# Optimization experiments

Hardware: AMD Instinct MI355X
Metric: run time of the kernel (lower is better)

The kernel has to match this reference:

```python
import jax, jax.numpy as jnp
import numpy as np

N = 100_000      # nodes
E = 1_600_000    # edges (avg degree 16)
D_IN = 128
D_H = 128
D_P = 128
D_OUT = 64


def setup_inputs() -> dict:
    key = jax.random.key(0)
    ks = jax.random.split(key, 10)
    x = jax.random.normal(ks[0], (N, D_IN), dtype=jnp.float32)
    edge_index = jax.random.randint(ks[1], (2, E), 0, N, dtype=jnp.int64)
    # Mix_Pass layer 0: Linear(in->hidden, bias=False) + separate bias (zero-init)
    W1 = jax.random.normal(ks[2], (D_H, D_IN), dtype=jnp.float32) * 0.05
    b1 = jnp.zeros((D_H,), dtype=jnp.float32)
    # Mix_Pass layer 1: hidden->hidden
    W2 = jax.random.normal(ks[3], (D_H, D_H), dtype=jnp.float32) * 0.05
    b2 = jnp.zeros((D_H,), dtype=jnp.float32)
    # projection MLP
    fcW1 = jax.random.normal(ks[4], (D_P, D_H), dtype=jnp.float32) * 0.05
    fcb1 = jnp.zeros((D_P,), dtype=jnp.float32)
    fcW2 = jax.random.normal(ks[5], (D_OUT, D_P), dtype=jnp.float32) * 0.05
    fcb2 = jnp.zeros((D_OUT,), dtype=jnp.float32)
    return dict(x=x, edge_index=edge_index, W1=W1, b1=b1, W2=W2, b2=b2,
                fcW1=fcW1, fcb1=fcb1, fcW2=fcW2, fcb2=fcb2)


def _gcn_norm_with_self_loops(edge_index, n_nodes):
    # add_self_loops then gcn_norm (sym, improved=False, loops already added)
    loop = jnp.arange(n_nodes, dtype=edge_index.dtype)
    row = jnp.concatenate([edge_index[0], loop])  # source
    col = jnp.concatenate([edge_index[1], loop])  # target
    ew = jnp.ones(row.shape[0], dtype=jnp.float32)
    deg = jax.ops.segment_sum(ew, col, num_segments=n_nodes)
    dinv = jnp.where(deg > 0, jax.lax.rsqrt(deg), 0.0)
    return row, col, dinv[row] * ew * dinv[col]


def _mix_pass(z, W, b, row, col, ew, n_nodes):
    z = z @ W.T                                   # [N, out]
    msg = ew[:, None] * z[row]                    # gather source feats, scale
    out = jax.ops.segment_sum(msg, col, num_segments=n_nodes)  # scatter-add
    return out + b


def reference(x, edge_index, W1, b1, W2, b2, fcW1, fcb1, fcW2, fcb2):
    n_nodes = x.shape[0]
    row, col, ew = _gcn_norm_with_self_loops(edge_index, n_nodes)
    # dropout is identity in eval mode
    z = jax.nn.relu(_mix_pass(x, W1, b1, row, col, ew, n_nodes))
    zs = _mix_pass(z, W2, b2, row, col, ew, n_nodes)
    # project: elu(fc1) -> log_softmax(fc2)
    h = jax.nn.elu(zs @ fcW1.T + fcb1)
    res = jax.nn.log_softmax(h @ fcW2.T + fcb2, axis=1)
    return zs, res
```

## Files before the change

### kernel.cpp

```cpp
#include <hip/hip_runtime.h>
#include <hip/hip_bf16.h>

typedef __bf16 bf16_t;
typedef bf16_t bf16x8 __attribute__((ext_vector_type(8)));
typedef bf16_t bf16x4 __attribute__((ext_vector_type(4)));
typedef bf16_t bf16x2 __attribute__((ext_vector_type(2)));
typedef float f32x4 __attribute__((ext_vector_type(4)));

#define DEG_CAP 64
#define BKT_SHIFT 8
#define BKT_CAP 6144
#define EPT 8

__device__ __forceinline__ void cvt4(const float* __restrict__ s, bf16_t* __restrict__ d, int i) {
    f32x4 v = ((const f32x4*)s)[i];
    bf16x4 o;
#pragma unroll
    for (int j = 0; j < 4; ++j) o[j] = (bf16_t)v[j];
    ((bf16x4*)d)[i] = o;
}

__global__ void setup_k(const float* xf, bf16_t* Xbf, int nx4,
                        const float* W1f, bf16_t* W1b,
                        const float* W2f, bf16_t* W2b,
                        const float* fW1f, bf16_t* fW1b,
                        const float* fW2f, bf16_t* fW2b,
                        int* gbcnt, int NB, int* yzero) {
    int i = blockIdx.x * blockDim.x + threadIdx.x;
    if (i < nx4) { cvt4(xf, Xbf, i); return; }
    i -= nx4;
    if (i < 4096) { cvt4(W1f, W1b, i); return; }
    i -= 4096;
    if (i < 4096) { cvt4(W2f, W2b, i); return; }
    i -= 4096;
    if (i < 4096) { cvt4(fW1f, fW1b, i); return; }
    i -= 4096;
    if (i < 2048) { cvt4(fW2f, fW2b, i); return; }
    i -= 2048;
    if (i < NB) { gbcnt[i] = 0; return; }
    i -= NB;
    if (i < 64) yzero[i] = 0;
}

__global__ __launch_bounds__(256) void bucket_scatter_k(const int* __restrict__ ei,
                                                        int* __restrict__ gbcnt,
                                                        unsigned* __restrict__ grec,
                                                        int E, int N) {
    __shared__ int hist[512];
    __shared__ int base[512];
    const int tid = threadIdx.x;
    const int NB = (N + 255) >> BKT_SHIFT;
    for (int i = tid; i < NB; i += 256) hist[i] = 0;
    __syncthreads();

    const int wave = tid >> 6, lane = tid & 63;
    const int e0 = blockIdx.x * (256 * EPT) + wave * (64 * EPT) + lane;
    const bool i64 = (ei[1] == 0) & (ei[3] == 0) & (ei[5] == 0) & (ei[7] == 0);

    unsigned rec[EPT];
    int lof[EPT];
    int bk[EPT];
#pragma unroll
    for (int j = 0; j < EPT; ++j) {
        int e = e0 + j * 64;
        bk[j] = -1;
        if (e < E) {
            int r, c;
            if (i64) { r = ei[2 * e]; c = ei[2 * E + 2 * e]; }
            else     { r = ei[e];     c = ei[E + e]; }
            r = ((unsigned)r < (unsigned)N) ? r : 0;
            c = ((unsigned)c < (unsigned)N) ? c : 0;
            int b = c >> BKT_SHIFT;
            rec[j] = ((unsigned)r << BKT_SHIFT) | (unsigned)(c & 255);
            bk[j] = b;
            lof[j] = atomicAdd(&hist[b], 1);
        }
    }
    __syncthreads();
    for (int i = tid; i < NB; i += 256)
        base[i] = hist[i] ? atomicAdd(&gbcnt[i], hist[i]) : 0;
    __syncthreads();
#pragma unroll
    for (int j = 0; j < EPT; ++j) {
        if (bk[j] >= 0) {
            int pos = base[bk[j]] + lof[j];
            if (pos < BKT_CAP)
                grec[(size_t)bk[j] * BKT_CAP + pos] = rec[j];
        }
    }
}

__global__ __launch_bounds__(256) void bucket_place_k(const int* __restrict__ gbcnt,
                                                      const unsigned* __restrict__ grec,
                                                      int* __restrict__ cnt,
                                                      int* __restrict__ srcx, int N) {
    __shared__ int lcnt[256];
    const int b = blockIdx.x, tid = threadIdx.x;
    lcnt[tid] = 0;
    __syncthreads();
    int ne = gbcnt[b];
    if (ne > BKT_CAP) ne = BKT_CAP;
    const unsigned* rp = grec + (size_t)b * BKT_CAP;
    const int node0 = b << BKT_SHIFT;
    for (int i = tid; i < ne; i += 256) {
        unsigned rec = rp[i];
        int cl = rec & 255;
        int r  = rec >> BKT_SHIFT;
        int p = atomicAdd(&lcnt[cl], 1);
        if (p < DEG_CAP) srcx[(size_t)(node0 + cl) * DEG_CAP + p] = r;
    }
    __syncthreads();
    int node = node0 + tid;
    if (node < N) {
        int c = lcnt[tid];
        cnt[node] = c;
        int cc = (c < DEG_CAP) ? c : DEG_CAP;
        int pe = (cc + 15) & ~15;
        if (pe > DEG_CAP) pe = DEG_CAP;
        int* s = srcx + (size_t)node * DEG_CAP;
        for (int p = cc; p < pe; ++p) s[p] = N;
    }
}

template <int RELU, int WF32>
__global__ __launch_bounds__(256) void gather_k(const bf16_t* __restrict__ Y,
                                                const int* __restrict__ cnt,
                                                const int* __restrict__ srcx,
                                                const float* __restrict__ bias,
                                                bf16_t* __restrict__ out,
                                                float* __restrict__ out2, int n) {
    int node0 = (blockIdx.x * 4 + (threadIdx.x >> 6)) * 2;
    if (node0 >= n) return;
    const int lane = threadIdx.x & 63;
    const int l16 = lane & 15;
    const int quad = lane >> 4;
    const bool has1 = node0 + 1 < n;
    const int node1 = has1 ? node0 + 1 : n;

    int2 cc = *(const int2*)(cnt + node0);
    int c0 = cc.x;
    int c1 = has1 ? cc.y : 0;
    float di0 = rsqrtf((float)c0 + 1.0f);
    float di1 = rsqrtf((float)c1 + 1.0f);
    int cg0 = (c0 < DEG_CAP) ? c0 : DEG_CAP;
    int cg1 = (c1 < DEG_CAP) ? c1 : DEG_CAP;
    int nb0 = (cg0 + 15) & ~15;
    int nb1 = (cg1 + 15) & ~15;
    int nbm = nb0 > nb1 ? nb0 : nb1;

    const int* sl0 = srcx + (size_t)node0 * DEG_CAP;
    const int* sl1 = srcx + (size_t)node1 * DEG_CAP;
    const bf16_t* Yl = Y + l16 * 8;

    bf16x8 ys0 = *(const bf16x8*)(Yl + (size_t)node0 * 128);
    bf16x8 ys1 = *(const bf16x8*)(Yl + (size_t)node1 * 128);

    float acc0[8], acc1[8];
#pragma unroll
    for (int j = 0; j < 8; ++j) { acc0[j] = 0.f; acc1[j] = 0.f; }

    for (int e = 0; e < nbm; e += 16) {
        int4 sq0, sq1;
        bool d0 = e < nb0, d1 = e < nb1;
        if (d0) sq0 = *(const int4*)(sl0 + e + quad * 4);
        if (d1) sq1 = *(const int4*)(sl1 + e + quad * 4);
        if (d0) {
            bf16x8 y0 = *(const bf16x8*)(Yl + (size_t)sq0.x * 128);
            bf16x8 y1 = *(const bf16x8*)(Yl + (size_t)sq0.y * 128);
            bf16x8 y2 = *(const bf16x8*)(Yl + (size_t)sq0.z * 128);
            bf16x8 y3 = *(const bf16x8*)(Yl + (size_t)sq0.w * 128);
#pragma unroll
            for (int j = 0; j < 8; ++j)
                acc0[j] += (float)y0[j] + (float)y1[j] + (float)y2[j] + (float)y3[j];
        }
        if (d1) {
            bf16x8 y0 = *(const bf16x8*)(Yl + (size_t)sq1.x * 128);
            bf16x8 y1 = *(const bf16x8*)(Yl + (size_t)sq1.y * 128);
            bf16x8 y2 = *(const bf16x8*)(Yl + (size_t)sq1.z * 128);
            bf16x8 y3 = *(const bf16x8*)(Yl + (size_t)sq1.w * 128);
#pragma unroll
            for (int j = 0; j < 8; ++j)
                acc1[j] += (float)y0[j] + (float)y1[j] + (float)y2[j] + (float)y3[j];
        }
    }

#pragma unroll
    for (int j = 0; j < 8; ++j) {
        acc0[j] += __shfl_xor(acc0[j], 16);
        acc0[j] += __shfl_xor(acc0[j], 32);
        acc1[j] += __shfl_xor(acc1[j], 16);
        acc1[j] += __shfl_xor(acc1[j], 32);
    }

    f32x4 b0 = ((const f32x4*)bias)[l16 * 2];
    f32x4 b1 = ((const f32x4*)bias)[l16 * 2 + 1];
    float v0[8], v1[8];
#pragma unroll
    for (int j = 0; j < 8; ++j) {
        float bb = (j < 4) ? b0[j & 3] : b1[j & 3];
        v0[j] = di0 * ((float)ys0[j] + acc0[j]) + bb;
        v1[j] = di1 * ((float)ys1[j] + acc1[j]) + bb;
        if (RELU) { v0[j] = fmaxf(v0[j], 0.f); v1[j] = fmaxf(v1[j], 0.f); }
    }

    if (quad == 0) {
        bf16x8 o;
#pragma unroll
        for (int j = 0; j < 8; ++j) o[j] = (bf16_t)v0[j];
        *(bf16x8*)(out + (size_t)node0 * 128 + l16 * 8) = o;
    } else if (quad == 1 && has1) {
        bf16x8 o;
#pragma unroll
        for (int j = 0; j < 8; ++j) o[j] = (bf16_t)v1[j];
        *(bf16x8*)(out + (size_t)node1 * 128 + l16 * 8) = o;
    }
    if (WF32) {
        if (quad == 2) {
            f32x4 w = {v0[0], v0[1], v0[2], v0[3]};
            *(f32x4*)(out2 + (size_t)node0 * 128 + l16 * 8) = w;
        } else if (quad == 3) {
            f32x4 w = {v0[4], v0[5], v0[6], v0[7]};
            *(f32x4*)(out2 + (size_t)node0 * 128 + l16 * 8 + 4) = w;
        } else if (quad == 0 && has1) {
            f32x4 w = {v1[0], v1[1], v1[2], v1[3]};
            *(f32x4*)(out2 + (size_t)node1 * 128 + l16 * 8) = w;
        } else if (quad == 1 && has1) {
            f32x4 w = {v1[4], v1[5], v1[6], v1[7]};
            *(f32x4*)(out2 + (size_t)node1 * 128 + l16 * 8 + 4) = w;
        }
    }
}

template <int OC, int MODE, int MT>
__global__ __launch_bounds__(256) void gemm_k(const bf16_t* __restrict__ A,
                                              const bf16_t* __restrict__ W,
                                              const float* __restrict__ bias,
                                              const int* __restrict__ cnt,
                                              bf16_t* __restrict__ out,
                                              float* __restrict__ outf, int nrows) {
    const int lane = threadIdx.x & 63;
    const int wave = threadIdx.x >> 6;
    const int l16 = lane & 15;
    const int quad = lane >> 4;
    constexpr int NT = OC / 16;
    const int ntiles = (nrows + 15) >> 4;
    const int t0 = (blockIdx.x * 4 + wave) * MT;
    if (t0 >= ntiles) return;

    f32x4 acc[MT][NT];
#pragma unroll
    for (int mt = 0; mt < MT; ++mt)
#pragma unroll
        for (int n = 0; n < NT; ++n) acc[mt][n] = (f32x4){0.f, 0.f, 0.f, 0.f};

    const bf16_t* arow[MT];
#pragma unroll
    for (int mt = 0; mt < MT; ++mt) {
        int r = t0 * 16 + mt * 16 + l16;
        if (r > nrows - 1) r = nrows - 1;
        arow[mt] = A + (size_t)r * 128 + quad * 8;
    }
    const bf16_t* wrow = W + (size_t)l16 * 128 + quad * 8;

#pragma unroll
    for (int kt = 0; kt < 4; ++kt) {
        bf16x8 a[MT];
#pragma unroll
        for (int mt = 0; mt < MT; ++mt) a[mt] = *(const bf16x8*)(arow[mt] + kt * 32);
#pragma unroll
        for (int n = 0; n < NT; ++n) {
            bf16x8 b = *(const bf16x8*)(wrow + (size_t)n * 2048 + kt * 32);
#pragma unroll
            for (int mt = 0; mt < MT; ++mt)
                acc[mt][n] = __builtin_amdgcn_mfma_f32_16x16x32_bf16(a[mt], b, acc[mt][n], 0, 0, 0);
        }
    }

#pragma unroll
    for (int mt = 0; mt < MT; ++mt) {
        int m0 = (t0 + mt) * 16;
        if (m0 >= nrows) break;
#pragma unroll
        for (int r = 0; r < 4; ++r) {
            int row = m0 + quad * 4 + r;
            if (row < nrows) {
                float sc = rsqrtf((float)cnt[row] + 1.0f);
#pragma unroll
                for (int n = 0; n < NT; ++n)
                    out[(size_t)row * OC + n * 16 + l16] = (bf16_t)(sc * acc[mt][n][r]);
            }
        }
    }
}

#define LDW 136
__global__ __launch_bounds__(256) void head_k(const bf16_t* __restrict__ A,
                                              const bf16_t* __restrict__ W1,
                                              const float* __restrict__ b1,
                                              const bf16_t* __restrict__ W2,
                                              const float* __restrict__ b2,
                                              float* __restrict__ outf, int nrows) {
    __shared__ bf16_t hl[4][16 * LDW];
    const int lane = threadIdx.x & 63;
    const int wave = threadIdx.x >> 6;
    const int l16 = lane & 15;
    const int quad = lane >> 4;
    const int ntiles = (nrows + 15) >> 4;
    int t = blockIdx.x * 4 + wave;
    const bool live = t < ntiles;
    if (!live) t = ntiles - 1;
    const int m0 = t * 16;

    f32x4 acc[8];
#pragma unroll
    for (int n = 0; n < 8; ++n) acc[n] = (f32x4){0.f, 0.f, 0.f, 0.f};
    int r0 = m0 + l16;
    if (r0 > nrows - 1) r0 = nrows - 1;
    const bf16_t* arow = A + (size_t)r0 * 128 + quad * 8;
    const bf16_t* wrow = W1 + (size_t)l16 * 128 + quad * 8;
#pragma unroll
    for (int kt = 0; kt < 4; ++kt) {
        bf16x8 a = *(const bf16x8*)(arow + kt * 32);
#pragma unroll
        for (int n = 0; n < 8; ++n) {
            bf16x8 b = *(const bf16x8*)(wrow + (size_t)n * 2048 + kt * 32);
            acc[n] = __builtin_amdgcn_mfma_f32_16x16x32_bf16(a, b, acc[n], 0, 0, 0);
        }
    }
    bf16_t* hw = hl[wave];
#pragma unroll
    for (int n = 0; n < 8; ++n) {
        float bb = b1[n * 16 + l16];
#pragma unroll
        for (int r = 0; r < 4; ++r) {
            float v = acc[n][r] + bb;
            v = (v > 0.0f) ? v : (expf(v) - 1.0f);
            hw[(quad * 4 + r) * LDW + n * 16 + l16] = (bf16_t)v;
        }
    }
    __syncthreads();

    f32x4 acc2[4];
#pragma unroll
    for (int n = 0; n < 4; ++n) acc2[n] = (f32x4){0.f, 0.f, 0.f, 0.f};
    const bf16_t* hrow = hw + l16 * LDW + quad * 8;
    const bf16_t* wrow2 = W2 + (size_t)l16 * 128 + quad * 8;
#pragma unroll
    for (int kt = 0; kt < 4; ++kt) {
        bf16x8 a = *(const bf16x8*)(hrow + kt * 32);
#pragma unroll
        for (int n = 0; n < 4; ++n) {
            bf16x8 b = *(const bf16x8*)(wrow2 + (size_t)n * 2048 + kt * 32);
            acc2[n] = __builtin_amdgcn_mfma_f32_16x16x32_bf16(a, b, acc2[n], 0, 0, 0);
        }
    }
#pragma unroll
    for (int r = 0; r < 4; ++r) {
        float v[4];
#pragma unroll
        for (int n = 0; n < 4; ++n) v[n] = acc2[n][r] + b2[n * 16 + l16];
        float mx = v[0];
#pragma unroll
        for (int n = 1; n < 4; ++n) mx = fmaxf(mx, v[n]);
#pragma unroll
        for (int m = 8; m >= 1; m >>= 1) mx = fmaxf(mx, __shfl_xor(mx, m));
        float s = 0.0f;
#pragma unroll
        for (int n = 0; n < 4; ++n) s += expf(v[n] - mx);
#pragma unroll
        for (int m = 8; m >= 1; m >>= 1) s += __shfl_xor(s, m);
        float lse = mx + logf(s);
        int row = m0 + quad * 4 + r;
        if (live && row < nrows)
#pragma unroll
            for (int n = 0; n < 4; ++n)
                outf[(size_t)row * 64 + n * 16 + l16] = v[n] - lse;
    }
}

extern "C" void kernel_launch(void* const* d_in, const int* in_sizes, int n_in,
                              void* d_out, int out_size, void* d_ws, size_t ws_size,
                              hipStream_t stream) {
    const float* xf    = (const float*)d_in[0];
    const int*   ei    = (const int*)d_in[1];
    const float* W1f   = (const float*)d_in[2];
    const float* b1f   = (const float*)d_in[3];
    const float* W2f   = (const float*)d_in[4];
    const float* b2f   = (const float*)d_in[5];
    const float* fcW1f = (const float*)d_in[6];
    const float* fcb1f = (const float*)d_in[7];
    const float* fcW2f = (const float*)d_in[8];
    const float* fcb2f = (const float*)d_in[9];

    const int N = in_sizes[0] / 128;
    const int E = in_sizes[1] / 2;
    const int NB = (N + 255) >> BKT_SHIFT;

    float* zs_out  = (float*)d_out;
    float* res_out = (float*)d_out + (size_t)N * 128;

    char* ws = (char*)d_ws;
    size_t o = 0;
    auto carve = [&](size_t bytes) { void* p = ws + o; o = (o + bytes + 255) & ~255UL; return p; };
    int*      cnt   = (int*)carve((size_t)N * 4);
    int*      srcx  = (int*)carve((size_t)N * DEG_CAP * 4);
    bf16_t*   Xbf   = (bf16_t*)carve((size_t)N * 128 * 2);
    bf16_t*   Ybf   = (bf16_t*)carve((size_t)(N + 1) * 128 * 2);
    bf16_t*   W1b   = (bf16_t*)carve(128 * 128 * 2);
    bf16_t*   W2b   = (bf16_t*)carve(128 * 128 * 2);
    bf16_t*   fW1b  = (bf16_t*)carve(128 * 128 * 2);
    bf16_t*   fW2b  = (bf16_t*)carve(64 * 128 * 2);
    unsigned* grec  = (unsigned*)carve((size_t)NB * BKT_CAP * 4);
    int*      gbcnt = (int*)carve((size_t)NB * 4);

    const int B = 256;
    const int ntiles = (N + 15) / 16;
    const int gblocks = (ntiles + 7) / 8;
    const int hblocks = (ntiles + 3) / 4;
    const int nodeblocks = (N + 7) / 8;
    const int nx4 = N * 32;
    const int nsetup = nx4 + 4096 * 3 + 2048 + NB + 64;
    const int ablocks = (E + 256 * EPT - 1) / (256 * EPT);

    setup_k<<<(nsetup + B - 1) / B, B, 0, stream>>>(xf, Xbf, nx4, W1f, W1b, W2f, W2b,
                                                    fcW1f, fW1b, fcW2f, fW2b, gbcnt, NB,
                                                    (int*)(Ybf + (size_t)N * 128));
    bucket_scatter_k<<<ablocks, B, 0, stream>>>(ei, gbcnt, grec, E, N);
    bucket_place_k<<<NB, B, 0, stream>>>(gbcnt, grec, cnt, srcx, N);

    gemm_k<128, 0, 2><<<gblocks, B, 0, stream>>>(Xbf, W1b, nullptr, cnt, Ybf, nullptr, N);
    gather_k<1, 0><<<nodeblocks, B, 0, stream>>>(Ybf, cnt, srcx, b1f, Xbf, nullptr, N);

    gemm_k<128, 0, 2><<<gblocks, B, 0, stream>>>(Xbf, W2b, nullptr, cnt, Ybf, nullptr, N);
    gather_k<0, 1><<<nodeblocks, B, 0, stream>>>(Ybf, cnt, srcx, b2f, Xbf, zs_out, N);

    head_k<<<hblocks, B, 0, stream>>>(Xbf, fW1b, fcb1f, fW2b, fcb2f, res_out, N);
}
```

Before: 417.2 us.

## Fuse x fp32-to-bf16 conversion into first GEMM and simplify gather to one node per wave

```diff
diff --git a/kernel.cpp b/kernel.cpp
--- a/kernel.cpp
+++ b/kernel.cpp
@@ -6,11 +6,12 @@
 typedef bf16_t bf16x4 __attribute__((ext_vector_type(4)));
 typedef bf16_t bf16x2 __attribute__((ext_vector_type(2)));
 typedef float f32x4 __attribute__((ext_vector_type(4)));
+typedef float f32x2 __attribute__((ext_vector_type(2)));
 
 #define DEG_CAP 64
 #define BKT_SHIFT 8
 #define BKT_CAP 6144
-#define EPT 8
+#define EPT 16
 
 __device__ __forceinline__ void cvt4(const float* __restrict__ s, bf16_t* __restrict__ d, int i) {
     f32x4 v = ((const f32x4*)s)[i];
@@ -20,15 +21,12 @@
     ((bf16x4*)d)[i] = o;
 }
 
-__global__ void setup_k(const float* xf, bf16_t* Xbf, int nx4,
-                        const float* W1f, bf16_t* W1b,
+__global__ void setup_k(const float* W1f, bf16_t* W1b,
                         const float* W2f, bf16_t* W2b,
                         const float* fW1f, bf16_t* fW1b,
                         const float* fW2f, bf16_t* fW2b,
                         int* gbcnt, int NB, int* yzero) {
     int i = blockIdx.x * blockDim.x + threadIdx.x;
-    if (i < nx4) { cvt4(xf, Xbf, i); return; }
-    i -= nx4;
     if (i < 4096) { cvt4(W1f, W1b, i); return; }
     i -= 4096;
     if (i < 4096) { cvt4(W2f, W2b, i); return; }
@@ -116,6 +114,7 @@
         cnt[node] = c;
         int cc = (c < DEG_CAP) ? c : DEG_CAP;
         int pe = (cc + 15) & ~15;
+        if (pe < 16) pe = 16;
         if (pe > DEG_CAP) pe = DEG_CAP;
         int* s = srcx + (size_t)node * DEG_CAP;
         for (int p = cc; p < pe; ++p) s[p] = N;
@@ -129,115 +128,87 @@
                                                 const float* __restrict__ bias,
                                                 bf16_t* __restrict__ out,
                                                 float* __restrict__ out2, int n) {
-    int node0 = (blockIdx.x * 4 + (threadIdx.x >> 6)) * 2;
-    if (node0 >= n) return;
+    int node = blockIdx.x * 4 + (threadIdx.x >> 6);
+    if (node >= n) return;
     const int lane = threadIdx.x & 63;
     const int l16 = lane & 15;
     const int quad = lane >> 4;
-    const bool has1 = node0 + 1 < n;
-    const int node1 = has1 ? node0 + 1 : n;
-
-    int2 cc = *(const int2*)(cnt + node0);
-    int c0 = cc.x;
-    int c1 = has1 ? cc.y : 0;
-    float di0 = rsqrtf((float)c0 + 1.0f);
-    float di1 = rsqrtf((float)c1 + 1.0f);
-    int cg0 = (c0 < DEG_CAP) ? c0 : DEG_CAP;
-    int cg1 = (c1 < DEG_CAP) ? c1 : DEG_CAP;
-    int nb0 = (cg0 + 15) & ~15;
-    int nb1 = (cg1 + 15) & ~15;
-    int nbm = nb0 > nb1 ? nb0 : nb1;
-
-    const int* sl0 = srcx + (size_t)node0 * DEG_CAP;
-    const int* sl1 = srcx + (size_t)node1 * DEG_CAP;
+    const int* sl = srcx + (size_t)node * DEG_CAP + quad * 4;
     const bf16_t* Yl = Y + l16 * 8;
 
-    bf16x8 ys0 = *(const bf16x8*)(Yl + (size_t)node0 * 128);
-    bf16x8 ys1 = *(const bf16x8*)(Yl + (size_t)node1 * 128);
-
-    float acc0[8], acc1[8];
-#pragma unroll
-    for (int j = 0; j < 8; ++j) { acc0[j] = 0.f; acc1[j] = 0.f; }
-
-    for (int e = 0; e < nbm; e += 16) {
-        int4 sq0, sq1;
-        bool d0 = e < nb0, d1 = e < nb1;
-        if (d0) sq0 = *(const int4*)(sl0 + e + quad * 4);
-        if (d1) sq1 = *(const int4*)(sl1 + e + quad * 4);
-        if (d0) {
-            bf16x8 y0 = *(const bf16x8*)(Yl + (size_t)sq0.x * 128);
-            bf16x8 y1 = *(const bf16x8*)(Yl + (size_t)sq0.y * 128);
-            bf16x8 y2 = *(const bf16x8*)(Yl + (size_t)sq0.z * 128);
-            bf16x8 y3 = *(const bf16x8*)(Yl + (size_t)sq0.w * 128);
-#pragma unroll
-            for (int j = 0; j < 8; ++j)
-                acc0[j] += (float)y0[j] + (float)y1[j] + (float)y2[j] + (float)y3[j];
-        }
-        if (d1) {
-            bf16x8 y0 = *(const bf16x8*)(Yl + (size_t)sq1.x * 128);
-            bf16x8 y1 = *(const bf16x8*)(Yl + (size_t)sq1.y * 128);
-            bf16x8 y2 = *(const bf16x8*)(Yl + (size_t)sq1.z * 128);
-            bf16x8 y3 = *(const bf16x8*)(Yl + (size_t)sq1.w * 128);
-#pragma unroll
-            for (int j = 0; j < 8; ++j)
-                acc1[j] += (float)y0[j] + (float)y1[j] + (float)y2[j] + (float)y3[j];
-        }
-    }
-
+    int4 sq = *(const int4*)sl;
+    bf16x8 ys = *(const bf16x8*)(Yl + (size_t)node * 128);
+    int c = cnt[node];
+    float di = rsqrtf((float)c + 1.0f);
+    int cg = (c < DEG_CAP) ? c : DEG_CAP;
+    int nb = (cg + 15) & ~15;
+
+    f32x2 acc[4];
+#pragma unroll
+    for (int p = 0; p < 4; ++p) acc[p] = (f32x2){0.f, 0.f};
+
+#define ACC_ROW(s)                                                             \
+    {                                                                          \
+        bf16x8 yv = *(const bf16x8*)(Yl + (size_t)(s) * 128);                  \
+        uint4 u = *(const uint4*)&yv;                                          \
+        acc[0] += (f32x2){__uint_as_float(u.x << 16),                          \
+                          __uint_as_float(u.x & 0xFFFF0000u)};                 \
+        acc[1] += (f32x2){__uint_as_float(u.y << 16),                          \
+                          __uint_as_float(u.y & 0xFFFF0000u)};                 \
+        acc[2] += (f32x2){__uint_as_float(u.z << 16),                          \
+                          __uint_as_float(u.z & 0xFFFF0000u)};                 \
+        acc[3] += (f32x2){__uint_as_float(u.w << 16),                          \
+                          __uint_as_float(u.w & 0xFFFF0000u)};                 \
+    }
+
+    ACC_ROW(sq.x); ACC_ROW(sq.y); ACC_ROW(sq.z); ACC_ROW(sq.w);
+    for (int e = 16; e < nb; e += 16) {
+        int4 s2 = *(const int4*)(sl + e);
+        ACC_ROW(s2.x); ACC_ROW(s2.y); ACC_ROW(s2.z); ACC_ROW(s2.w);
+    }
+#undef ACC_ROW
+
+    float a[8];
+#pragma unroll
+    for (int p = 0; p < 4; ++p) { a[2 * p] = acc[p][0]; a[2 * p + 1] = acc[p][1]; }
 #pragma unroll
     for (int j = 0; j < 8; ++j) {
-        acc0[j] += __shfl_xor(acc0[j], 16);
-        acc0[j] += __shfl_xor(acc0[j], 32);
-        acc1[j] += __shfl_xor(acc1[j], 16);
-        acc1[j] += __shfl_xor(acc1[j], 32);
+        a[j] += __shfl_xor(a[j], 16);
+        a[j] += __shfl_xor(a[j], 32);
     }
 
     f32x4 b0 = ((const f32x4*)bias)[l16 * 2];
     f32x4 b1 = ((const f32x4*)bias)[l16 * 2 + 1];
-    float v0[8], v1[8];
+    float v[8];
 #pragma unroll
     for (int j = 0; j < 8; ++j) {
         float bb = (j < 4) ? b0[j & 3] : b1[j & 3];
-        v0[j] = di0 * ((float)ys0[j] + acc0[j]) + bb;
-        v1[j] = di1 * ((float)ys1[j] + acc1[j]) + bb;
-        if (RELU) { v0[j] = fmaxf(v0[j], 0.f); v1[j] = fmaxf(v1[j], 0.f); }
+        v[j] = di * ((float)ys[j] + a[j]) + bb;
+        if (RELU) v[j] = fmaxf(v[j], 0.f);
     }
 
     if (quad == 0) {
         bf16x8 o;
 #pragma unroll
-        for (int j = 0; j < 8; ++j) o[j] = (bf16_t)v0[j];
-        *(bf16x8*)(out + (size_t)node0 * 128 + l16 * 8) = o;
-    } else if (quad == 1 && has1) {
-        bf16x8 o;
-#pragma unroll
-        for (int j = 0; j < 8; ++j) o[j] = (bf16_t)v1[j];
-        *(bf16x8*)(out + (size_t)node1 * 128 + l16 * 8) = o;
+        for (int j = 0; j < 8; ++j) o[j] = (bf16_t)v[j];
+        *(bf16x8*)(out + (size_t)node * 128 + l16 * 8) = o;
     }
     if (WF32) {
-        if (quad == 2) {
-            f32x4 w = {v0[0], v0[1], v0[2], v0[3]};
-            *(f32x4*)(out2 + (size_t)node0 * 128 + l16 * 8) = w;
-        } else if (quad == 3) {
-            f32x4 w = {v0[4], v0[5], v0[6], v0[7]};
-            *(f32x4*)(out2 + (size_t)node0 * 128 + l16 * 8 + 4) = w;
-        } else if (quad == 0 && has1) {
-            f32x4 w = {v1[0], v1[1], v1[2], v1[3]};
-            *(f32x4*)(out2 + (size_t)node1 * 128 + l16 * 8) = w;
-        } else if (quad == 1 && has1) {
-            f32x4 w = {v1[4], v1[5], v1[6], v1[7]};
-            *(f32x4*)(out2 + (size_t)node1 * 128 + l16 * 8 + 4) = w;
-        }
-    }
-}
-
-template <int OC, int MODE, int MT>
-__global__ __launch_bounds__(256) void gemm_k(const bf16_t* __restrict__ A,
+        if (quad == 1) {
+            f32x4 w = {v[0], v[1], v[2], v[3]};
+            *(f32x4*)(out2 + (size_t)node * 128 + l16 * 8) = w;
+        } else if (quad == 2) {
+            f32x4 w = {v[4], v[5], v[6], v[7]};
+            *(f32x4*)(out2 + (size_t)node * 128 + l16 * 8 + 4) = w;
+        }
+    }
+}
+
+template <int OC, int MT, int AF32>
+__global__ __launch_bounds__(256) void gemm_k(const void* __restrict__ Av,
                                               const bf16_t* __restrict__ W,
-                                              const float* __restrict__ bias,
                                               const int* __restrict__ cnt,
-                                              bf16_t* __restrict__ out,
-                                              float* __restrict__ outf, int nrows) {
+                                              bf16_t* __restrict__ out, int nrows) {
     const int lane = threadIdx.x & 63;
     const int wave = threadIdx.x >> 6;
     const int l16 = lane & 15;
@@ -254,11 +225,13 @@
         for (int n = 0; n < NT; ++n) acc[mt][n] = (f32x4){0.f, 0.f, 0.f, 0.f};
 
     const bf16_t* arow[MT];
+    const float* afrow[MT];
 #pragma unroll
     for (int mt = 0; mt < MT; ++mt) {
         int r = t0 * 16 + mt * 16 + l16;
         if (r > nrows - 1) r = nrows - 1;
-        arow[mt] = A + (size_t)r * 128 + quad * 8;
+        if (AF32) afrow[mt] = (const float*)Av + (size_t)r * 128 + quad * 8;
+        else      arow[mt]  = (const bf16_t*)Av + (size_t)r * 128 + quad * 8;
     }
     const bf16_t* wrow = W + (size_t)l16 * 128 + quad * 8;
 
@@ -266,7 +239,19 @@
     for (int kt = 0; kt < 4; ++kt) {
         bf16x8 a[MT];
 #pragma unroll
-        for (int mt = 0; mt < MT; ++mt) a[mt] = *(const bf16x8*)(arow[mt] + kt * 32);
+        for (int mt = 0; mt < MT; ++mt) {
+            if (AF32) {
+                f32x4 lo = *(const f32x4*)(afrow[mt] + kt * 32);
+                f32x4 hi = *(const f32x4*)(afrow[mt] + kt * 32 + 4);
+#pragma unroll
+                for (int j = 0; j < 4; ++j) {
+                    a[mt][j] = (bf16_t)lo[j];
+                    a[mt][j + 4] = (bf16_t)hi[j];
+                }
+            } else {
+                a[mt] = *(const bf16x8*)(arow[mt] + kt * 32);
+            }
+        }
 #pragma unroll
         for (int n = 0; n < NT; ++n) {
             bf16x8 b = *(const bf16x8*)(wrow + (size_t)n * 2048 + kt * 32);
@@ -417,21 +402,20 @@
     const int ntiles = (N + 15) / 16;
     const int gblocks = (ntiles + 7) / 8;
     const int hblocks = (ntiles + 3) / 4;
-    const int nodeblocks = (N + 7) / 8;
-    const int nx4 = N * 32;
-    const int nsetup = nx4 + 4096 * 3 + 2048 + NB + 64;
+    const int nodeblocks = (N + 3) / 4;
+    const int nsetup = 4096 * 3 + 2048 + NB + 64;
     const int ablocks = (E + 256 * EPT - 1) / (256 * EPT);
 
-    setup_k<<<(nsetup + B - 1) / B, B, 0, stream>>>(xf, Xbf, nx4, W1f, W1b, W2f, W2b,
+    setup_k<<<(nsetup + B - 1) / B, B, 0, stream>>>(W1f, W1b, W2f, W2b,
                                                     fcW1f, fW1b, fcW2f, fW2b, gbcnt, NB,
                                                     (int*)(Ybf + (size_t)N * 128));
     bucket_scatter_k<<<ablocks, B, 0, stream>>>(ei, gbcnt, grec, E, N);
     bucket_place_k<<<NB, B, 0, stream>>>(gbcnt, grec, cnt, srcx, N);
 
-    gemm_k<128, 0, 2><<<gblocks, B, 0, stream>>>(Xbf, W1b, nullptr, cnt, Ybf, nullptr, N);
+    gemm_k<128, 2, 1><<<gblocks, B, 0, stream>>>((const void*)xf, W1b, cnt, Ybf, N);
     gather_k<1, 0><<<nodeblocks, B, 0, stream>>>(Ybf, cnt, srcx, b1f, Xbf, nullptr, N);
 
-    gemm_k<128, 0, 2><<<gblocks, B, 0, stream>>>(Xbf, W2b, nullptr, cnt, Ybf, nullptr, N);
+    gemm_k<128, 2, 0><<<gblocks, B, 0, stream>>>((const void*)Xbf, W2b, cnt, Ybf, N);
     gather_k<0, 1><<<nodeblocks, B, 0, stream>>>(Ybf, cnt, srcx, b2f, Xbf, zs_out, N);
 
     head_k<<<hblocks, B, 0, stream>>>(Xbf, fW1b, fcb1f, fW2b, fcb2f, res_out, N);
```

Measured after the change: 394.6 us. 1.06x faster.
